# Optimization experiments

Hardware: AMD Instinct MI355X
Metric: run time of the kernel (lower is better)

## Reference

```python
import jax, jax.numpy as jnp
import numpy as np

DIM = 1024
H = 16
HKV = 4
HD = DIM // H  # 64
GROUP = H // HKV
ROPE_BASE = 10000.0
B, T = 2, 2048


def rms_norm(x, eps):
    return x * jax.lax.rsqrt(jnp.mean(x * x, axis=-1, keepdims=True) + eps)


def apply_rotary(x, cos, sin):
    # x: [B, h, T, HD]; cos/sin: [1, 1, T, HD//2]
    half = x.shape[-1] // 2
    x1, x2 = x[..., :half], x[..., half:]
    return jnp.concatenate([x1 * cos + x2 * sin, -x1 * sin + x2 * cos], axis=-1)


def setup_inputs() -> dict:
    key = jax.random.key(0)
    ks = jax.random.split(key, 5)
    s = 0.02
    return {
        "x": jax.random.normal(ks[0], (B, T, DIM), dtype=jnp.float32),
        "Wq": jax.random.normal(ks[1], (DIM, DIM), dtype=jnp.float32) * s,
        "Wk": jax.random.normal(ks[2], (HKV * HD, DIM), dtype=jnp.float32) * s,
        "Wv": jax.random.normal(ks[3], (HKV * HD, DIM), dtype=jnp.float32) * s,
        "Wproj": jax.random.normal(ks[4], (DIM, DIM), dtype=jnp.float32) * s,
        "q_gain": jnp.full((H,), 12.0, dtype=jnp.float32),
    }


def reference(x, Wq, Wk, Wv, Wproj, q_gain):
    bsz, seqlen, dim = x.shape
    eps = jnp.asarray(jnp.finfo(x.dtype).eps, x.dtype)

    # double RMSNorm path: normalized input for q/k, raw input for v
    x_qk = rms_norm(x, eps)
    q = (x_qk @ Wq.T).reshape(bsz, seqlen, H, HD).transpose(0, 2, 1, 3)    # [B,H,T,D]
    k = (x_qk @ Wk.T).reshape(bsz, seqlen, HKV, HD).transpose(0, 2, 1, 3)  # [B,Hkv,T,D]
    v = (x @ Wv.T).reshape(bsz, seqlen, HKV, HD).transpose(0, 2, 1, 3)     # [B,Hkv,T,D]

    q = rms_norm(q, eps)
    k = rms_norm(k, eps)

    # rotary embeddings
    t = jnp.arange(seqlen, dtype=jnp.float32)
    inv_freq = 1.0 / (ROPE_BASE ** (jnp.arange(0, HD, 2, dtype=jnp.float32) / HD))
    freqs = jnp.outer(t, inv_freq)                       # [T, HD//2]
    cos = jnp.cos(freqs)[None, None].astype(x.dtype)
    sin = jnp.sin(freqs)[None, None].astype(x.dtype)
    q = apply_rotary(q, cos, sin)
    k = apply_rotary(k, cos, sin)

    # per-head gain on q
    q = q * q_gain.astype(q.dtype)[None, :, None, None]

    # GQA: expand kv heads to query heads
    k_r = jnp.repeat(k, GROUP, axis=1)  # [B,H,T,D]
    v_r = jnp.repeat(v, GROUP, axis=1)

    scale = 1.0 / np.sqrt(HD)
    scores = jnp.einsum("bhqd,bhkd->bhqk", q, k_r) * scale
    causal = jnp.tril(jnp.ones((seqlen, seqlen), dtype=bool))
    scores = jnp.where(causal[None, None], scores, jnp.asarray(-jnp.inf, scores.dtype))
    attn = jax.nn.softmax(scores, axis=-1)
    y = jnp.einsum("bhqk,bhkd->bhqd", attn, v_r)          # [B,H,T,D]

    # XSA: remove value-direction component from output
    y_bt = y.transpose(0, 2, 1, 3)                        # [B,T,H,D]
    v_bt = v.transpose(0, 2, 1, 3)                        # [B,T,Hkv,D]
    y_g = y_bt.reshape(bsz, seqlen, HKV, GROUP, HD)
    vnorm = jnp.sqrt(jnp.sum(v_bt * v_bt, axis=-1, keepdims=True))
    vn = (v_bt / jnp.maximum(vnorm, 1e-12))[..., None, :]  # [B,T,Hkv,1,D]
    proj = jnp.sum(y_g * vn, axis=-1, keepdims=True) * vn
    y_bt = (y_g - proj).reshape(bsz, seqlen, H, HD)

    return y_bt.reshape(bsz, seqlen, dim) @ Wproj.T
```

## Files before the change

kernel.cpp:

```cpp
#include <hip/hip_runtime.h>
#include <hip/hip_bf16.h>

typedef __attribute__((ext_vector_type(8))) short bf8v;
typedef __attribute__((ext_vector_type(4))) float f4v;
typedef __attribute__((ext_vector_type(4))) unsigned u4v;

#define MFMA16(a,b,c) __builtin_amdgcn_mfma_f32_16x16x32_bf16((a),(b),(c),0,0,0)

#define GLD16(gp, lp) __builtin_amdgcn_global_load_lds( \
    (const __attribute__((address_space(1))) void*)(gp), \
    (__attribute__((address_space(3))) void*)(lp), 16, 0, 0)

#define DIMC   1024
#define TSEQ   2048
#define NH     16
#define NKV    4
#define HDIM   64
#define RMS_EPS 1.1920929e-07f
#define QSCALE 0.1803368801111601f

__device__ __forceinline__ ushort f2bf(float f) {
  unsigned u = __builtin_bit_cast(unsigned, f);
  u = (u + 0x7FFFu + ((u >> 16) & 1u)) >> 16;
  return (ushort)u;
}
__device__ __forceinline__ float bf2f(ushort u) {
  return __builtin_bit_cast(float, (unsigned)u << 16);
}
__device__ __forceinline__ unsigned cvtpk(float lo, float hi) {
  unsigned r;
  asm("v_cvt_pk_bf16_f32 %0, %1, %2" : "=v"(r) : "v"(lo), "v"(hi));
  return r;
}

__global__ __launch_bounds__(256) void prep_all(
    const float* __restrict__ x,
    const float* __restrict__ Wq, const float* __restrict__ Wk,
    const float* __restrict__ Wv, const float* __restrict__ Wp,
    ushort* __restrict__ xhi, ushort* __restrict__ xlo,
    ushort* __restrict__ xb,
    ushort* __restrict__ wqkh, ushort* __restrict__ wqkl,
    ushort* __restrict__ wvb, ushort* __restrict__ wpb,
    float* __restrict__ cosT, float* __restrict__ sinT) {
  __shared__ float red[4];
  int bid = blockIdx.x, tid = threadIdx.x;
  if (bid < 4096) {
    int row = bid;
    int lane = tid & 63, w = tid >> 6;
    float4 v = ((const float4*)(x + (size_t)row * DIMC))[tid];
    float ss = v.x * v.x + v.y * v.y + v.z * v.z + v.w * v.w;
    for (int off = 32; off; off >>= 1) ss += __shfl_xor(ss, off);
    if (lane == 0) red[w] = ss;
    __syncthreads();
    float tot = red[0] + red[1] + red[2] + red[3];
    float rs = rsqrtf(tot * (1.0f / DIMC) + RMS_EPS);
    float n0 = v.x * rs, n1 = v.y * rs, n2 = v.z * rs, n3 = v.w * rs;
    ushort4 h, l, ob;
    h.x = f2bf(n0); l.x = f2bf(n0 - bf2f(h.x));
    h.y = f2bf(n1); l.y = f2bf(n1 - bf2f(h.y));
    h.z = f2bf(n2); l.z = f2bf(n2 - bf2f(h.z));
    h.w = f2bf(n3); l.w = f2bf(n3 - bf2f(h.w));
    ob.x = f2bf(v.x); ob.y = f2bf(v.y); ob.z = f2bf(v.z); ob.w = f2bf(v.w);
    ((ushort4*)(xhi + (size_t)row * DIMC))[tid] = h;
    ((ushort4*)(xlo + (size_t)row * DIMC))[tid] = l;
    ((ushort4*)(xb  + (size_t)row * DIMC))[tid] = ob;
    return;
  }
  int wb = bid - 4096;
  if (wb < 1280) {
    const float* src;
    size_t si, di;
    if (wb < 1024) { src = Wq; si = (size_t)wb * 256 + tid; di = si; }
    else { src = Wk; si = (size_t)(wb - 1024) * 256 + tid; di = 262144 + si; }
    float4 v = ((const float4*)src)[si];
    ushort4 h, l;
    h.x = f2bf(v.x); l.x = f2bf(v.x - bf2f(h.x));
    h.y = f2bf(v.y); l.y = f2bf(v.y - bf2f(h.y));
    h.z = f2bf(v.z); l.z = f2bf(v.z - bf2f(h.z));
    h.w = f2bf(v.w); l.w = f2bf(v.w - bf2f(h.w));
    ((ushort4*)wqkh)[di] = h;
    ((ushort4*)wqkl)[di] = l;
  } else if (wb < 2560) {
    const float* src;
    ushort* dst;
    int i;
    if (wb < 1536) { src = Wv; dst = wvb; i = (wb - 1280) * 256 + tid; }
    else           { src = Wp; dst = wpb; i = (wb - 1536) * 256 + tid; }
    float4 v = ((const float4*)src)[i];
    ushort4 o;
    o.x = f2bf(v.x); o.y = f2bf(v.y); o.z = f2bf(v.z); o.w = f2bf(v.w);
    ((ushort4*)dst)[i] = o;
  } else {
    int i = (wb - 2560) * 256 + tid;
    int t = i >> 5, j = i & 31;
    float inv = 1.0f / powf(10000.0f, (float)j * (1.0f / 32.0f));
    float f = (float)t * inv;
    cosT[i] = cosf(f);
    sinT[i] = sinf(f);
  }
}

__global__ __launch_bounds__(256, 3)
void gemm_qkv(const ushort* __restrict__ xhi, const ushort* __restrict__ xlo,
              const ushort* __restrict__ wqkh, const ushort* __restrict__ wqkl,
              float* __restrict__ QKf, ushort* __restrict__ QKc,
              const ushort* __restrict__ xb, const ushort* __restrict__ wvb,
              float* __restrict__ Vf) {
  __shared__ __align__(16) ushort lA[128 * 64];
  __shared__ __align__(16) ushort lB[128 * 64];
  const int bid = blockIdx.x;
  int u;
  bool big;
  if (bid < 256)      { big = true;  u = bid; }
  else if (bid < 448) { big = false; u = bid - 256; }
  else if (bid < 512) { big = true;  u = 256 + (bid - 448); }
  else                { big = false; u = 192 + (bid - 512); }

  const ushort *Ap0, *Bp0, *Ap1, *Bp1;
  float* Cf = QKf;
  int N = 1280, nsteps, mt, n0;
  if (big) {
    mt = u / 10; n0 = (u % 10) * 128;
    Ap0 = xlo; Bp0 = wqkh; Ap1 = xhi; Bp1 = wqkl; nsteps = 32;
  } else if (u < 320) {
    mt = u / 10; n0 = (u % 10) * 128;
    Ap0 = xhi; Bp0 = wqkh; Ap1 = Ap0; Bp1 = Bp0; nsteps = 16;
  } else {
    int v = u - 320; mt = v >> 1; n0 = (v & 1) * 128;
    Ap0 = xb; Bp0 = wvb; Ap1 = Ap0; Bp1 = Bp0; nsteps = 16;
    Cf = Vf; N = 256;
  }
  const int m0 = mt * 128;

  const int t = threadIdx.x;
  const int lane = t & 63, w = t >> 6;
  const int wr = w >> 1, wc = w & 1;
  const int l15 = lane & 15, lg = lane >> 4;
  const int srow = t >> 3, scp = t & 7;

  f4v acc[4][4] = {};

  for (int s = 0; s < nsteps; ++s) {
    const ushort* Ab = (s < 16) ? Ap0 : Ap1;
    const ushort* Bb = (s < 16) ? Bp0 : Bp1;
    const int kk = (s & 15) * 64;
    for (int i = 0; i < 4; ++i) {
      int row = srow + i * 32;
      int sc = scp ^ (row & 7);
      const ushort* ga = Ab + (size_t)(m0 + row) * DIMC + kk + sc * 8;
      const ushort* gb = Bb + (size_t)(n0 + row) * DIMC + kk + sc * 8;
      GLD16(ga, &lA[w * 512 + i * 2048]);
      GLD16(gb, &lB[w * 512 + i * 2048]);
    }
    __syncthreads();
    for (int kx = 0; kx < 2; ++kx) {
      bf8v af[4], bfr[4];
      for (int m = 0; m < 4; ++m) {
        int row = wr * 64 + m * 16 + l15;
        int ch = (kx * 4 + lg) ^ (row & 7);
        af[m] = *(const bf8v*)&lA[row * 64 + ch * 8];
      }
      for (int n = 0; n < 4; ++n) {
        int row = wc * 64 + n * 16 + l15;
        int ch = (kx * 4 + lg) ^ (row & 7);
        bfr[n] = *(const bf8v*)&lB[row * 64 + ch * 8];
      }
      for (int m = 0; m < 4; ++m)
        for (int n = 0; n < 4; ++n)
          acc[m][n] = MFMA16(af[m], bfr[n], acc[m][n]);
    }
    __syncthreads();
  }

  if (big) {
    for (int m = 0; m < 4; ++m)
      for (int n = 0; n < 4; ++n)
        for (int j = 0; j < 4; ++j) {
          int r = m0 + wr * 64 + m * 16 + lg * 4 + j;
          int c = n0 + wc * 64 + n * 16 + l15;
          QKc[(size_t)r * 1280 + c] = f2bf(acc[m][n][j]);
        }
  } else {
    for (int m = 0; m < 4; ++m)
      for (int n = 0; n < 4; ++n)
        for (int j = 0; j < 4; ++j) {
          int r = m0 + wr * 64 + m * 16 + lg * 4 + j;
          int c = n0 + wc * 64 + n * 16 + l15;
          Cf[(size_t)r * N + c] = acc[m][n][j];
        }
  }
}

__global__ __launch_bounds__(256, 2)
void gemm_bt(const ushort* __restrict__ A0, const ushort* __restrict__ B0,
             float* __restrict__ C, int N) {
  __shared__ __align__(16) ushort lA[128 * 64];
  __shared__ __align__(16) ushort lB[64 * 64];
  const int t = threadIdx.x;
  const int lane = t & 63, w = t >> 6;
  const int l15 = lane & 15, lg = lane >> 4;
  const int m0 = blockIdx.y * 128, n0 = blockIdx.x * 64;
  const int srow = t >> 3, scp = t & 7;

  f4v acc[2][4] = {};

  for (int k0 = 0; k0 < 1024; k0 += 64) {
    for (int i = 0; i < 4; ++i) {
      int row = srow + i * 32;
      int sc = scp ^ (row & 7);
      const ushort* ga = A0 + (size_t)(m0 + row) * DIMC + k0 + sc * 8;
      GLD16(ga, &lA[w * 512 + i * 2048]);
    }
    for (int i = 0; i < 2; ++i) {
      int row = srow + i * 32;
      int sc = scp ^ (row & 7);
      const ushort* gb = B0 + (size_t)(n0 + row) * DIMC + k0 + sc * 8;
      GLD16(gb, &lB[w * 512 + i * 2048]);
    }
    __syncthreads();
    for (int kx = 0; kx < 2; ++kx) {
      bf8v af[2], bfr[4];
      for (int m = 0; m < 2; ++m) {
        int row = w * 32 + m * 16 + l15;
        int ch = (kx * 4 + lg) ^ (row & 7);
        af[m] = *(const bf8v*)&lA[row * 64 + ch * 8];
      }
      for (int n = 0; n < 4; ++n) {
        int row = n * 16 + l15;
        int ch = (kx * 4 + lg) ^ (row & 7);
        bfr[n] = *(const bf8v*)&lB[row * 64 + ch * 8];
      }
      for (int m = 0; m < 2; ++m)
        for (int n = 0; n < 4; ++n)
          acc[m][n] = MFMA16(af[m], bfr[n], acc[m][n]);
    }
    __syncthreads();
  }

  for (int m = 0; m < 2; ++m)
    for (int n = 0; n < 4; ++n)
      for (int j = 0; j < 4; ++j) {
        int r = m0 + w * 32 + m * 16 + lg * 4 + j;
        int c = n0 + n * 16 + l15;
        C[(size_t)r * N + c] = acc[m][n][j];
      }
}

__global__ __launch_bounds__(256) void post_all(
    const float* __restrict__ QKf, const ushort* __restrict__ QKc,
    const float* __restrict__ cosT,
    const float* __restrict__ sinT, const float* __restrict__ qgain,
    ushort* __restrict__ qhi, ushort* __restrict__ qlo,
    ushort* __restrict__ kb16,
    const float* __restrict__ Vf, ushort* __restrict__ vt2,
    ushort* __restrict__ vhat_q) {
  __shared__ float lds[64][69];
  __shared__ float rnv[64];
  int bid = blockIdx.x;
  if (bid < 4096) {
    int m = bid;
    int b = m >> 11, tpos = m & 2047;
    int lane = threadIdx.x & 63, w = threadIdx.x >> 6;
    int d = lane, j = d & 31;
    float sgn = (d < 32) ? 1.0f : -1.0f;
    float c = cosT[tpos * 32 + j], s = sinT[tpos * 32 + j];

    for (int i = 0; i < 4; ++i) {
      int h = w * 4 + i;
      size_t base = (size_t)m * 1280 + h * HDIM + d;
      float q = QKf[base] + bf2f(QKc[base]);
      float ss = q * q;
      for (int off = 32; off; off >>= 1) ss += __shfl_xor(ss, off);
      float rs = rsqrtf(ss * (1.0f / HDIM) + RMS_EPS);
      float qn = q * rs;
      float partner = __shfl_xor(qn, 32);
      float ro = (qn * c + sgn * partner * s) * (qgain[h] * QSCALE);
      ushort hi = f2bf(ro);
      ushort lo = f2bf(ro - bf2f(hi));
      size_t idx = (((size_t)b * NH + h) * TSEQ + tpos) * HDIM + d;
      qhi[idx] = hi;
      qlo[idx] = lo;
    }
    {
      int kv = w;
      size_t base = (size_t)m * 1280 + 1024 + kv * HDIM + d;
      float k = QKf[base] + bf2f(QKc[base]);
      float ss = k * k;
      for (int off = 32; off; off >>= 1) ss += __shfl_xor(ss, off);
      float rs = rsqrtf(ss * (1.0f / HDIM) + RMS_EPS);
      float kn = k * rs;
      float partner = __shfl_xor(kn, 32);
      float ro = kn * c + sgn * partner * s;
      kb16[((size_t)(b * NKV + kv) * TSEQ + tpos) * HDIM + d] = f2bf(ro);
    }
    return;
  }
  {
    int vb = bid - 4096;
    int bkv = vb >> 5, tt = vb & 31;
    int b = bkv >> 2, kv = bkv & 3;
    int tid = threadIdx.x;
    for (int i = 0; i < 16; ++i) {
      int idx = i * 256 + tid;
      int tloc = idx >> 6, d = idx & 63;
      lds[d][tloc] = Vf[((size_t)(b * TSEQ + tt * 64 + tloc)) * 256 + kv * 64 + d];
    }
    __syncthreads();
    {
      int t = tid >> 2, prt = tid & 3;
      float ssum = 0.f;
      for (int dd = 0; dd < 16; ++dd) {
        float v = lds[prt * 16 + dd][t];
        ssum += v * v;
      }
      ssum += __shfl_xor(ssum, 1);
      ssum += __shfl_xor(ssum, 2);
      if (prt == 0) rnv[t] = 1.0f / fmaxf(sqrtf(ssum), 1e-12f);
    }
    __syncthreads();
    for (int i = 0; i < 16; ++i) {
      int idx = i * 256 + tid;
      int d = idx >> 6, tloc = idx & 63;
      vt2[(size_t)bkv * (TSEQ * 64) + tt * 4096 + d * 64 + tloc] = f2bf(lds[d][tloc]);
    }
    for (int i = 0; i < 16; ++i) {
      int idx = i * 256 + tid;
      int tloc = idx >> 6, d = idx & 63;
      vhat_q[((size_t)bkv * TSEQ + tt * 64 + tloc) * 64 + d] =
          f2bf(lds[d][tloc] * rnv[tloc]);
    }
  }
}

#define E(s,t,k,l) ((unsigned)(s) | ((unsigned)(t) << 8) | \
                    ((unsigned)(k) << 16) | ((unsigned)(l) << 24))
__global__ __launch_bounds__(256, 5) void attn_chunk(
    const ushort* __restrict__ qhi, const ushort* __restrict__ qlo,
    const ushort* __restrict__ kb16, const ushort* __restrict__ vt2,
    ushort* __restrict__ pyb, float* __restrict__ pml) {
  static const unsigned LUT[80] = {
    E(76,31,0,8), E(77,31,8,8), E(78,31,16,8), E(79,31,24,8),
    E(72,30,0,8), E(73,30,8,8), E(74,30,16,8),
    E(68,29,0,8), E(69,29,8,8), E(64,28,0,8),
    E(45,23,0,8), E(46,23,8,8), E(47,23,16,8),
    E(42,22,0,8), E(43,22,8,8), E(39,21,0,8),
    E(22,15,0,8), E(23,15,8,8), E(20,14,0,8), E(7,7,0,8),
    E(75,30,24,7), E(70,29,16,7), E(71,29,23,7),
    E(65,28,8,7), E(66,28,15,7), E(67,28,22,7),
    E(60,27,0,7), E(61,27,7,7), E(62,27,14,7), E(63,27,21,7),
    E(56,26,0,7), E(57,26,7,7), E(58,26,14,7),
    E(52,25,0,7), E(53,25,7,7), E(48,24,0,7),
    E(44,22,16,7), E(40,21,8,7), E(41,21,15,7),
    E(36,20,0,7), E(37,20,7,7), E(38,20,14,7),
    E(33,19,0,7), E(34,19,7,7), E(30,18,0,7),
    E(21,14,8,7), E(18,13,0,7), E(19,13,7,7), E(16,12,0,7), E(6,6,0,7),
    E(59,26,21,6), E(54,25,14,6), E(55,25,20,6),
    E(49,24,7,6), E(50,24,13,6), E(51,24,19,6),
    E(35,19,14,6), E(31,18,7,6), E(32,18,13,6),
    E(27,17,0,6), E(28,17,6,6), E(29,17,12,6),
    E(24,16,0,6), E(25,16,6,6),
    E(17,12,7,6), E(14,11,0,6), E(15,11,6,6), E(12,10,0,6), E(5,5,0,6),
    E(26,16,12,5), E(13,10,6,5), E(10,9,0,5), E(11,9,5,5),
    E(8,8,0,5), E(4,4,0,5),
    E(9,8,5,4), E(3,3,0,4),
    E(2,2,0,3), E(1,1,0,2), E(0,0,0,1)
  };
  __shared__ __align__(16) ushort lk[2][64 * 64];
  __shared__ __align__(16) ushort lv[2][64 * 64];
  const int t = threadIdx.x;
  const int lane = t & 63, w = t >> 6;
  const int bid = blockIdx.x;
  const int combo = bid & 31;
  const unsigned e = LUT[bid >> 5];
  const int slot = e & 255;
  const int tile = (e >> 8) & 31;
  const int kb0 = (e >> 16) & 31;
  const int len = (int)(e >> 24);

  const int xcd = combo & 7, g = (combo >> 3) & 3;
  const int b = xcd >> 2, kv = xcd & 3, h = kv * 4 + g;
  const int l15 = lane & 15, lg = lane >> 4;
  const int q0 = tile * 64 + w * 16;
  const int t3 = t >> 3, tc8 = t & 7;
  const int rx = l15 & 7;
  const bool odd = (lg & 1);

  const size_t qoff = (((size_t)(b * NH + h)) * TSEQ + q0 + l15) * HDIM;
  bf8v bq0h = *(const bf8v*)(qhi + qoff + lg * 8);
  bf8v bq1h = *(const bf8v*)(qhi + qoff + 32 + lg * 8);
  bf8v bq0l = *(const bf8v*)(qlo + qoff + lg * 8);
  bf8v bq1l = *(const bf8v*)(qlo + qoff + 32 + lg * 8);

  const ushort* kb = kb16 + (size_t)(b * NKV + kv) * TSEQ * 64;
  const ushort* vb = vt2 + (size_t)(b * NKV + kv) * TSEQ * 64;

#define STAGE(BUF, KT) do { \
    _Pragma("unroll") \
    for (int i = 0; i < 2; ++i) { \
      int row = i * 32 + t3; \
      int sc = tc8 ^ (row & 7); \
      GLD16(kb + (size_t)((KT) * 64 + row) * 64 + sc * 8, \
            &lk[BUF][(i * 32 + (w << 3)) * 64]); \
      GLD16(vb + (size_t)(KT) * 4096 + row * 64 + sc * 8, \
            &lv[BUF][(i * 32 + (w << 3)) * 64]); \
    } } while (0)

  STAGE(0, kb0);

  f4v y[4] = {};
  f4v lsum = {};
  float mrow = 0.f;
  const short ob16 = (short)0x3F80;
  const bf8v onesv = { ob16, ob16, ob16, ob16, ob16, ob16, ob16, ob16 };

#pragma unroll 1
  for (int itc = 0; itc < len; ++itc) {
    const int cur = itc & 1;
    const int kt = kb0 + itc;
    __syncthreads();
    if (itc + 1 < len) STAGE(cur ^ 1, kt + 1);

    const ushort* lkc = &lk[cur][0];
    const ushort* lvc = &lv[cur][0];
    const int kv0 = kt * 64;

    f4v s4[4];
    const f4v zi = { -mrow, -mrow, -mrow, -mrow };
    __builtin_amdgcn_s_setprio(1);
#pragma unroll
    for (int n = 0; n < 4; ++n) {
      const ushort* krow = lkc + (n * 16 + l15) * 64;
      bf8v kh0 = *(const bf8v*)&krow[((0 + lg) ^ rx) * 8];
      bf8v kh1 = *(const bf8v*)&krow[((4 + lg) ^ rx) * 8];
      f4v acc = MFMA16(kh0, bq0h, zi);
      acc = MFMA16(kh1, bq1h, acc);
      acc = MFMA16(kh0, bq0l, acc);
      acc = MFMA16(kh1, bq1l, acc);
      s4[n] = acc;
    }
    __builtin_amdgcn_s_setprio(0);

    const bool need_mask = (kt == tile);
    float mloc = -1e30f;
#pragma unroll
    for (int n = 0; n < 4; ++n)
#pragma unroll
      for (int j = 0; j < 4; ++j) {
        float v = s4[n][j];
        if (need_mask && (kv0 + n * 16 + lg * 4 + j > q0 + l15)) v = -1e30f;
        s4[n][j] = v;
        mloc = fmaxf(mloc, v);
      }
    if (__any(mloc > 11.5f)) {
      float mf = fmaxf(mloc, __shfl_xor(mloc, 16));
      mf = fmaxf(mf, __shfl_xor(mf, 32));
      float delta = fmaxf(mf, 0.f);
      float scf = exp2f(-delta);
      lsum *= scf;
#pragma unroll
      for (int n = 0; n < 4; ++n) y[n] *= scf;
#pragma unroll
      for (int n = 0; n < 4; ++n)
#pragma unroll
        for (int j = 0; j < 4; ++j) s4[n][j] -= delta;
      mrow += delta;
    }
#pragma unroll
    for (int n = 0; n < 4; ++n)
#pragma unroll
      for (int j = 0; j < 4; ++j)
        s4[n][j] = exp2f(s4[n][j]);

    unsigned d0a = cvtpk(s4[0][0], s4[0][1]), d0b = cvtpk(s4[0][2], s4[0][3]);
    unsigned d1a = cvtpk(s4[1][0], s4[1][1]), d1b = cvtpk(s4[1][2], s4[1][3]);
    unsigned d2a = cvtpk(s4[2][0], s4[2][1]), d2b = cvtpk(s4[2][2], s4[2][3]);
    unsigned d3a = cvtpk(s4[3][0], s4[3][1]), d3b = cvtpk(s4[3][2], s4[3][3]);
    asm("v_permlane32_swap_b32 %0, %1" : "+v"(d0a), "+v"(d1a));
    asm("v_permlane32_swap_b32 %0, %1" : "+v"(d0b), "+v"(d1b));
    asm("v_permlane32_swap_b32 %0, %1" : "+v"(d2a), "+v"(d3a));
    asm("v_permlane32_swap_b32 %0, %1" : "+v"(d2b), "+v"(d3b));
    unsigned sa0 = (unsigned)__shfl_xor((int)d0a, 16);
    unsigned sb0 = (unsigned)__shfl_xor((int)d1a, 16);
    unsigned sa1 = (unsigned)__shfl_xor((int)d0b, 16);
    unsigned sb1 = (unsigned)__shfl_xor((int)d1b, 16);
    unsigned sa2 = (unsigned)__shfl_xor((int)d2a, 16);
    unsigned sb2 = (unsigned)__shfl_xor((int)d3a, 16);
    unsigned sa3 = (unsigned)__shfl_xor((int)d2b, 16);
    unsigned sb3 = (unsigned)__shfl_xor((int)d3b, 16);
    u4v u0 = { odd ? sb0 : d0a, odd ? sb1 : d0b,
               odd ? d1a : sa0, odd ? d1b : sa1 };
    u4v u1 = { odd ? sb2 : d2a, odd ? sb3 : d2b,
               odd ? d3a : sa2, odd ? d3b : sa3 };
    bf8v pb0 = __builtin_bit_cast(bf8v, u0);
    bf8v pb1 = __builtin_bit_cast(bf8v, u1);

    __builtin_amdgcn_s_setprio(1);
#pragma unroll
    for (int n = 0; n < 4; ++n) {
      const ushort* vrow = lvc + (n * 16 + l15) * 64;
      bf8v va0 = *(const bf8v*)&vrow[((0 + lg) ^ rx) * 8];
      bf8v va1 = *(const bf8v*)&vrow[((4 + lg) ^ rx) * 8];
      y[n] = MFMA16(va0, pb0, y[n]);
      y[n] = MFMA16(va1, pb1, y[n]);
    }
    lsum = MFMA16(onesv, pb0, lsum);
    lsum = MFMA16(onesv, pb1, lsum);
    __builtin_amdgcn_s_setprio(0);
  }
#undef STAGE

  {
    const float lrow = lsum[0];
    const int pslot = combo * 80 + slot;
    ushort* pb = pyb + (size_t)pslot * 4096;
    const int q = w * 16 + l15;
#pragma unroll
    for (int n = 0; n < 4; ++n) {
      uint2 pk;
      pk.x = cvtpk(y[n][0], y[n][1]);
      pk.y = cvtpk(y[n][2], y[n][3]);
      *(uint2*)&pb[q * 64 + n * 16 + lg * 4] = pk;
    }
    if (lane < 16) {
      float* mlp = pml + (size_t)pslot * 128;
      mlp[q] = mrow;
      mlp[64 + q] = lrow;
    }
  }
}
#undef E

__global__ __launch_bounds__(256) void combine_kern(
    const ushort* __restrict__ pyb, const float* __restrict__ pml,
    const ushort* __restrict__ vhat_q, ushort* __restrict__ ytil) {
  const int bid = blockIdx.x;
  const int combo = bid & 31, tile = bid >> 5;
  const int xcd = combo & 7, g = (combo >> 3) & 3;
  const int b = xcd >> 2, kv = xcd & 3, h = kv * 4 + g;
  const int nch = (tile + 8) >> 3;
  const int sb = (tile < 8) ? tile
               : (tile < 16) ? 8 + ((tile - 8) << 1)
               : (tile < 24) ? 24 + 3 * (tile - 16)
                             : 48 + ((tile - 24) << 2);
  const int tid = threadIdx.x;
  const int q = tid >> 2, ds = (tid & 3) * 16;
  const int q0 = tile * 64;

  float m[4], l[4];
#pragma unroll
  for (int ci = 0; ci < 4; ++ci) {
    if (ci < nch) {
      const float* mlp = pml + (size_t)(combo * 80 + sb + ci) * 128;
      m[ci] = mlp[q];
      l[ci] = mlp[64 + q];
    } else { m[ci] = -1e30f; l[ci] = 0.f; }
  }
  float M = fmaxf(fmaxf(m[0], m[1]), fmaxf(m[2], m[3]));
  float y[16] = {};
  float ltot = 0.f;
#pragma unroll
  for (int ci = 0; ci < 4; ++ci) {
    if (ci < nch) {
      float sc = exp2f(m[ci] - M);
      ltot += l[ci] * sc;
      const ushort* pb = pyb + (size_t)(combo * 80 + sb + ci) * 4096 + q * 64 + ds;
      bf8v p0 = *(const bf8v*)pb;
      bf8v p1 = *(const bf8v*)(pb + 8);
#pragma unroll
      for (int dd = 0; dd < 8; ++dd) {
        y[dd] += sc * bf2f((ushort)p0[dd]);
        y[8 + dd] += sc * bf2f((ushort)p1[dd]);
      }
    }
  }
  float inv = 1.0f / fmaxf(ltot, 1e-37f);
  const ushort* vh = vhat_q + ((size_t)(b * NKV + kv) * TSEQ + q0 + q) * 64 + ds;
  bf8v v0 = *(const bf8v*)vh;
  bf8v v1 = *(const bf8v*)(vh + 8);
  float vv[16];
  float dp = 0.f;
#pragma unroll
  for (int dd = 0; dd < 8; ++dd) {
    vv[dd] = bf2f((ushort)v0[dd]);
    vv[8 + dd] = bf2f((ushort)v1[dd]);
  }
#pragma unroll
  for (int dd = 0; dd < 16; ++dd) {
    y[dd] *= inv;
    dp += y[dd] * vv[dd];
  }
  dp += __shfl_xor(dp, 1);
  dp += __shfl_xor(dp, 2);
  bf8v o0, o1;
#pragma unroll
  for (int dd = 0; dd < 8; ++dd) {
    o0[dd] = (short)f2bf(y[dd] - dp * vv[dd]);
    o1[dd] = (short)f2bf(y[8 + dd] - dp * vv[8 + dd]);
  }
  ushort* yo = ytil + ((size_t)(b * TSEQ + q0 + q)) * DIMC + h * HDIM + ds;
  *(bf8v*)yo = o0;
  *(bf8v*)(yo + 8) = o1;
}

extern "C" void kernel_launch(void* const* d_in, const int* in_sizes, int n_in,
                              void* d_out, int out_size, void* d_ws, size_t ws_size,
                              hipStream_t stream) {
  (void)in_sizes; (void)n_in; (void)out_size; (void)ws_size;
  const float* x  = (const float*)d_in[0];
  const float* Wq = (const float*)d_in[1];
  const float* Wk = (const float*)d_in[2];
  const float* Wv = (const float*)d_in[3];
  const float* Wp = (const float*)d_in[4];
  const float* qg = (const float*)d_in[5];
  float* out = (float*)d_out;
  char* ws = (char*)d_ws;
  const size_t KB = 1024, MB = 1ull << 20;

  ushort* xhi = (ushort*)(ws);
  ushort* xlo = (ushort*)(ws + 8 * MB);
  ushort* xb  = (ushort*)(ws + 16 * MB);
  ushort* wqkh = (ushort*)(ws + 24 * MB);
  ushort* wqkl = (ushort*)(ws + 26 * MB + 512 * KB);
  ushort* wvb = (ushort*)(ws + 29 * MB);
  ushort* wpb = (ushort*)(ws + 29 * MB + 512 * KB);
  float*  cosT = (float*)(ws + 31 * MB + 512 * KB);
  float*  sinT = (float*)(ws + 31 * MB + 768 * KB);
  float*  QKf  = (float*)(ws + 32 * MB);
  ushort* kb16 = (ushort*)(ws + 52 * MB);
  ushort* vt2  = (ushort*)(ws + 54 * MB);

  float*  Vf   = out;
  ushort* QKc  = (ushort*)((char*)out + 4 * MB);
  ushort* vhat_q = (ushort*)((char*)out + 14 * MB);
  ushort* qhb  = xhi;
  ushort* qlb  = xlo;
  ushort* ytil = xb;
  ushort* pyb = (ushort*)(ws + 32 * MB);
  float*  pml = (float*)(ws + 56 * MB);

  prep_all<<<6912, 256, 0, stream>>>(x, Wq, Wk, Wv, Wp, xhi, xlo, xb,
                                     wqkh, wqkl, wvb, wpb, cosT, sinT);

  gemm_qkv<<<704, 256, 0, stream>>>(xhi, xlo, wqkh, wqkl, QKf, QKc,
                                    xb, wvb, Vf);

  post_all<<<4352, 256, 0, stream>>>(QKf, QKc, cosT, sinT, qg, qhb, qlb, kb16,
                                     Vf, vt2, vhat_q);
  attn_chunk<<<2560, 256, 0, stream>>>(qhb, qlb, kb16, vt2, pyb, pml);
  combine_kern<<<1024, 256, 0, stream>>>(pyb, pml, vhat_q, ytil);
  gemm_bt<<<dim3(16, 32), 256, 0, stream>>>(ytil, wpb, out, 1024);
}
```

Measured before the change: 140.6 us.

## Triple-buffer QKV GEMM loads and shrink output-projection GEMM tiles

The QKV GEMM now uses three LDS buffers with two stages prefetched ahead, waiting on vmcnt and a single barrier per step so global-to-LDS loads overlap MFMA work. The output projection GEMM drops its tile from 128x64 to 64x64 and doubles the grid to 1024 blocks, with higher occupancy bounds, so more blocks can run across the CUs. The triple buffering triples LDS use for gemm_qkv to 96KB, which may lower occupancy. The smaller projection tiles cut per-block data reuse.

```diff
diff --git a/kernel.cpp b/kernel.cpp
--- a/kernel.cpp
+++ b/kernel.cpp
@@ -106,8 +106,8 @@
               float* __restrict__ QKf, ushort* __restrict__ QKc,
               const ushort* __restrict__ xb, const ushort* __restrict__ wvb,
               float* __restrict__ Vf) {
-  __shared__ __align__(16) ushort lA[128 * 64];
-  __shared__ __align__(16) ushort lB[128 * 64];
+  __shared__ __align__(16) ushort lA[3][128 * 64];
+  __shared__ __align__(16) ushort lB[3][128 * 64];
   const int bid = blockIdx.x;
   int u;
   bool big;
@@ -140,37 +140,54 @@
 
   f4v acc[4][4] = {};
 
+#define QSTAGE(BUF, S) do { \
+    const ushort* Ab_ = ((S) < 16) ? Ap0 : Ap1; \
+    const ushort* Bb_ = ((S) < 16) ? Bp0 : Bp1; \
+    const int kk_ = ((S) & 15) * 64; \
+    _Pragma("unroll") \
+    for (int i = 0; i < 4; ++i) { \
+      int row = srow + i * 32; \
+      int sc = scp ^ (row & 7); \
+      GLD16(Ab_ + (size_t)(m0 + row) * DIMC + kk_ + sc * 8, \
+            &lA[BUF][w * 512 + i * 2048]); \
+      GLD16(Bb_ + (size_t)(n0 + row) * DIMC + kk_ + sc * 8, \
+            &lB[BUF][w * 512 + i * 2048]); \
+    } } while (0)
+
+  QSTAGE(0, 0);
+  QSTAGE(1, 1);
+
+  int cur = 0;
+#pragma unroll 1
   for (int s = 0; s < nsteps; ++s) {
-    const ushort* Ab = (s < 16) ? Ap0 : Ap1;
-    const ushort* Bb = (s < 16) ? Bp0 : Bp1;
-    const int kk = (s & 15) * 64;
-    for (int i = 0; i < 4; ++i) {
-      int row = srow + i * 32;
-      int sc = scp ^ (row & 7);
-      const ushort* ga = Ab + (size_t)(m0 + row) * DIMC + kk + sc * 8;
-      const ushort* gb = Bb + (size_t)(n0 + row) * DIMC + kk + sc * 8;
-      GLD16(ga, &lA[w * 512 + i * 2048]);
-      GLD16(gb, &lB[w * 512 + i * 2048]);
-    }
-    __syncthreads();
+    if (s + 1 < nsteps) asm volatile("s_waitcnt vmcnt(8)" ::: "memory");
+    else                asm volatile("s_waitcnt vmcnt(0)" ::: "memory");
+    __builtin_amdgcn_s_barrier();
+    if (s + 2 < nsteps) {
+      int nxt = cur + 2; if (nxt >= 3) nxt -= 3;
+      QSTAGE(nxt, s + 2);
+    }
+    const ushort* la = &lA[cur][0];
+    const ushort* lb = &lB[cur][0];
     for (int kx = 0; kx < 2; ++kx) {
       bf8v af[4], bfr[4];
       for (int m = 0; m < 4; ++m) {
         int row = wr * 64 + m * 16 + l15;
         int ch = (kx * 4 + lg) ^ (row & 7);
-        af[m] = *(const bf8v*)&lA[row * 64 + ch * 8];
+        af[m] = *(const bf8v*)&la[row * 64 + ch * 8];
       }
       for (int n = 0; n < 4; ++n) {
         int row = wc * 64 + n * 16 + l15;
         int ch = (kx * 4 + lg) ^ (row & 7);
-        bfr[n] = *(const bf8v*)&lB[row * 64 + ch * 8];
+        bfr[n] = *(const bf8v*)&lb[row * 64 + ch * 8];
       }
       for (int m = 0; m < 4; ++m)
         for (int n = 0; n < 4; ++n)
           acc[m][n] = MFMA16(af[m], bfr[n], acc[m][n]);
     }
-    __syncthreads();
-  }
+    cur = cur + 1; if (cur >= 3) cur = 0;
+  }
+#undef QSTAGE
 
   if (big) {
     for (int m = 0; m < 4; ++m)
@@ -191,59 +208,49 @@
   }
 }
 
-__global__ __launch_bounds__(256, 2)
+__global__ __launch_bounds__(256, 4)
 void gemm_bt(const ushort* __restrict__ A0, const ushort* __restrict__ B0,
              float* __restrict__ C, int N) {
-  __shared__ __align__(16) ushort lA[128 * 64];
+  __shared__ __align__(16) ushort lA[64 * 64];
   __shared__ __align__(16) ushort lB[64 * 64];
   const int t = threadIdx.x;
   const int lane = t & 63, w = t >> 6;
   const int l15 = lane & 15, lg = lane >> 4;
-  const int m0 = blockIdx.y * 128, n0 = blockIdx.x * 64;
+  const int m0 = blockIdx.y * 64, n0 = blockIdx.x * 64;
   const int srow = t >> 3, scp = t & 7;
 
-  f4v acc[2][4] = {};
+  f4v acc[4] = {};
 
   for (int k0 = 0; k0 < 1024; k0 += 64) {
-    for (int i = 0; i < 4; ++i) {
-      int row = srow + i * 32;
-      int sc = scp ^ (row & 7);
-      const ushort* ga = A0 + (size_t)(m0 + row) * DIMC + k0 + sc * 8;
-      GLD16(ga, &lA[w * 512 + i * 2048]);
-    }
     for (int i = 0; i < 2; ++i) {
       int row = srow + i * 32;
       int sc = scp ^ (row & 7);
-      const ushort* gb = B0 + (size_t)(n0 + row) * DIMC + k0 + sc * 8;
-      GLD16(gb, &lB[w * 512 + i * 2048]);
+      GLD16(A0 + (size_t)(m0 + row) * DIMC + k0 + sc * 8,
+            &lA[w * 512 + i * 2048]);
+      GLD16(B0 + (size_t)(n0 + row) * DIMC + k0 + sc * 8,
+            &lB[w * 512 + i * 2048]);
     }
     __syncthreads();
     for (int kx = 0; kx < 2; ++kx) {
-      bf8v af[2], bfr[4];
-      for (int m = 0; m < 2; ++m) {
-        int row = w * 32 + m * 16 + l15;
-        int ch = (kx * 4 + lg) ^ (row & 7);
-        af[m] = *(const bf8v*)&lA[row * 64 + ch * 8];
-      }
+      int arow = w * 16 + l15;
+      int ach = (kx * 4 + lg) ^ (arow & 7);
+      bf8v af = *(const bf8v*)&lA[arow * 64 + ach * 8];
       for (int n = 0; n < 4; ++n) {
         int row = n * 16 + l15;
         int ch = (kx * 4 + lg) ^ (row & 7);
-        bfr[n] = *(const bf8v*)&lB[row * 64 + ch * 8];
+        bf8v bfr = *(const bf8v*)&lB[row * 64 + ch * 8];
+        acc[n] = MFMA16(af, bfr, acc[n]);
       }
-      for (int m = 0; m < 2; ++m)
-        for (int n = 0; n < 4; ++n)
-          acc[m][n] = MFMA16(af[m], bfr[n], acc[m][n]);
     }
     __syncthreads();
   }
 
-  for (int m = 0; m < 2; ++m)
-    for (int n = 0; n < 4; ++n)
-      for (int j = 0; j < 4; ++j) {
-        int r = m0 + w * 32 + m * 16 + lg * 4 + j;
-        int c = n0 + n * 16 + l15;
-        C[(size_t)r * N + c] = acc[m][n][j];
-      }
+  for (int n = 0; n < 4; ++n)
+    for (int j = 0; j < 4; ++j) {
+      int r = m0 + w * 16 + lg * 4 + j;
+      int c = n0 + n * 16 + l15;
+      C[(size_t)r * N + c] = acc[n][j];
+    }
 }
 
 __global__ __launch_bounds__(256) void post_all(
@@ -648,5 +655,5 @@
                                      Vf, vt2, vhat_q);
   attn_chunk<<<2560, 256, 0, stream>>>(qhb, qlb, kb16, vt2, pyb, pml);
   combine_kern<<<1024, 256, 0, stream>>>(pyb, pml, vhat_q, ytil);
-  gemm_bt<<<dim3(16, 32), 256, 0, stream>>>(ytil, wpb, out, 1024);
-}
+  gemm_bt<<<dim3(16, 64), 256, 0, stream>>>(ytil, wpb, out, 1024);
+}
```

New measurement: 167.8 us. +19.3%, slower.
